# Kernel tuning notes

Hardware: AMD Instinct MI355X
Metric: run time of the kernel (lower is better)

The kernel has to match this reference:

```python
import jax, jax.numpy as jnp
import numpy as np

IN_FEATURES = 512
OUT_FEATURES = 64
INTER = 16
BATCH = 512


def setup_inputs() -> dict:
    key = jax.random.key(0)
    kx, kt = jax.random.split(key)
    x = jax.random.normal(kx, (BATCH, IN_FEATURES), dtype=jnp.float32)
    T = jax.random.normal(kt, (IN_FEATURES, OUT_FEATURES * INTER), dtype=jnp.float32)
    return {"x": x, "T": T}


def reference(x, T):
    B = x.shape[0]
    # M: [B, out, inter]
    M = (x @ T).reshape(B, OUT_FEATURES, INTER)
    # pairwise L1 distance over the intermediate dim: [B, B, out]
    l1 = jnp.sum(jnp.abs(M[:, None, :, :] - M[None, :, :, :]), axis=3)
    sim = jnp.exp(-l1)
    mask = 1.0 - jnp.eye(B, dtype=x.dtype)[:, :, None]  # exclude self
    o_b = jnp.sum(sim * mask, axis=1)  # [B, out]
    return jnp.concatenate([x, o_b], axis=1)
```

## Files before the change

### kernel.cpp

```cpp
#include <hip/hip_runtime.h>

#define IN_F 512
#define OUT_F 64
#define MCOLS 1024
#define OUT_STRIDE 576

__global__ __launch_bounds__(256) void gemm_init_kernel(
    const float* __restrict__ x, const float* __restrict__ T,
    float* __restrict__ M, float* __restrict__ out)
{
    __shared__ float xs[32][33];
    __shared__ float ts[32][64];

    const int tid = threadIdx.x;
    const int tx = tid & 15;
    const int ty = tid >> 4;
    const int c0 = blockIdx.x * 64;
    const int r0 = blockIdx.y * 32;

    float acc[2][4] = {{0.f,0.f,0.f,0.f},{0.f,0.f,0.f,0.f}};

    for (int kc = 0; kc < IN_F; kc += 32) {
        {
            const int ii = tid >> 3;
            const int kq = tid & 7;
            const float4 v = *(const float4*)(x + (r0 + ii) * IN_F + kc + kq * 4);
            xs[kq*4+0][ii] = v.x;
            xs[kq*4+1][ii] = v.y;
            xs[kq*4+2][ii] = v.z;
            xs[kq*4+3][ii] = v.w;
        }
        {
            const int jq = tid & 15;
#pragma unroll
            for (int h = 0; h < 2; ++h) {
                const int kk = (tid >> 4) + h * 16;
                const float4 v = *(const float4*)(T + (size_t)(kc + kk) * MCOLS + c0 + jq * 4);
                *(float4*)&ts[kk][jq * 4] = v;
            }
        }
        __syncthreads();
#pragma unroll
        for (int kk = 0; kk < 32; ++kk) {
            const float a0 = xs[kk][ty*2 + 0];
            const float a1 = xs[kk][ty*2 + 1];
            const float4 b = *(const float4*)&ts[kk][tx * 4];
            acc[0][0] += a0 * b.x; acc[0][1] += a0 * b.y;
            acc[0][2] += a0 * b.z; acc[0][3] += a0 * b.w;
            acc[1][0] += a1 * b.x; acc[1][1] += a1 * b.y;
            acc[1][2] += a1 * b.z; acc[1][3] += a1 * b.w;
        }
        __syncthreads();
    }

#pragma unroll
    for (int u = 0; u < 2; ++u) {
        const float4 w = make_float4(acc[u][0], acc[u][1], acc[u][2], acc[u][3]);
        *(float4*)(M + (size_t)(r0 + ty*2 + u) * MCOLS + c0 + tx * 4) = w;
    }

    const int bid = blockIdx.y * 16 + blockIdx.x;
    {
        const int idx = (bid * 256 + tid) * 4;
        const int i = idx >> 9;
        const int c = idx & 511;
        *(float4*)(out + (size_t)i * OUT_STRIDE + c) = *(const float4*)(x + idx);
    }
    if (tid < 128) {
        const int idx = bid * 128 + tid;
        const int i = idx >> 6;
        const int o = idx & 63;
        out[(size_t)i * OUT_STRIDE + IN_F + o] = -1.0f;
    }
}

__global__ __launch_bounds__(256) void pairwise_kernel(
    const float* __restrict__ M, float* __restrict__ out)
{
    __shared__ float sj[8 * 1024];

    const int tid = threadIdx.x;
    const int o  = tid & 63;
    const int ig = tid >> 6;
    const int it = blockIdx.x & 31;
    const int jc = blockIdx.x >> 5;
    const int i0 = it * 16;
    const int j0 = jc * 32;

    float mi[4][16];
#pragma unroll
    for (int r = 0; r < 4; ++r) {
        const float* rowp = M + (size_t)(i0 + ig*4 + r) * MCOLS + o * 16;
#pragma unroll
        for (int q = 0; q < 4; ++q) {
            const float4 v = *(const float4*)(rowp + q * 4);
            mi[r][q*4+0] = v.x; mi[r][q*4+1] = v.y;
            mi[r][q*4+2] = v.z; mi[r][q*4+3] = v.w;
        }
    }

    float acc[4] = {0.f, 0.f, 0.f, 0.f};

    const int ko = 4 * (tid & 3);
    const int oo = tid >> 2;

    for (int jb = 0; jb < 32; jb += 8) {
#pragma unroll
        for (int q = 0; q < 8; ++q) {
            const float4 v = *(const float4*)(M + (size_t)(j0 + jb + q) * MCOLS + tid * 4);
            float* s = sj + q * 1024 + oo;
            s[(ko+0)*64] = v.x;
            s[(ko+1)*64] = v.y;
            s[(ko+2)*64] = v.z;
            s[(ko+3)*64] = v.w;
        }
        __syncthreads();
#pragma unroll
        for (int q = 0; q < 8; ++q) {
            const float* s = sj + q * 1024 + o;
            float vj[16];
#pragma unroll
            for (int k = 0; k < 16; ++k) vj[k] = s[k * 64];
#pragma unroll
            for (int r = 0; r < 4; ++r) {
                float l1 = 0.f;
#pragma unroll
                for (int k = 0; k < 16; ++k) l1 += fabsf(mi[r][k] - vj[k]);
                acc[r] += __expf(-l1);
            }
        }
        __syncthreads();
    }

#pragma unroll
    for (int r = 0; r < 4; ++r) {
        atomicAdd(out + (size_t)(i0 + ig*4 + r) * OUT_STRIDE + IN_F + o, acc[r]);
    }
}

extern "C" void kernel_launch(void* const* d_in, const int* in_sizes, int n_in,
                              void* d_out, int out_size, void* d_ws, size_t ws_size,
                              hipStream_t stream) {
    const float* x = (const float*)d_in[0];
    const float* T = (const float*)d_in[1];
    float* out = (float*)d_out;
    float* M = (float*)d_ws;

    dim3 gridA(16, 16);
    gemm_init_kernel<<<gridA, 256, 0, stream>>>(x, T, M, out);
    pairwise_kernel<<<512, 256, 0, stream>>>(M, out);
}
```

Before: 98.25 us.

## Use bf16 MFMA GEMM with pre-transposed T and retile pairwise kernel

Measured after the change: 83.86 us. 14.6% less time.

```diff
diff --git a/kernel.cpp b/kernel.cpp
--- a/kernel.cpp
+++ b/kernel.cpp
@@ -1,141 +1,162 @@
 #include <hip/hip_runtime.h>
 
-#define IN_F 512
-#define OUT_F 64
-#define MCOLS 1024
 #define OUT_STRIDE 576
 
-__global__ __launch_bounds__(256) void gemm_init_kernel(
-    const float* __restrict__ x, const float* __restrict__ T,
-    float* __restrict__ M, float* __restrict__ out)
+typedef __attribute__((ext_vector_type(8))) short bf16x8;
+typedef __attribute__((ext_vector_type(4))) float f32x4;
+
+__device__ inline unsigned short f2bf(float f) {
+    unsigned u = __float_as_uint(f);
+    u = (u + 0x7FFFu + ((u >> 16) & 1u)) >> 16;
+    return (unsigned short)u;
+}
+
+__global__ __launch_bounds__(256) void transpose_T_kernel(
+    const float* __restrict__ T, unsigned short* __restrict__ Tb)
 {
-    __shared__ float xs[32][33];
-    __shared__ float ts[32][64];
-
-    const int tid = threadIdx.x;
-    const int tx = tid & 15;
-    const int ty = tid >> 4;
-    const int c0 = blockIdx.x * 64;
-    const int r0 = blockIdx.y * 32;
-
-    float acc[2][4] = {{0.f,0.f,0.f,0.f},{0.f,0.f,0.f,0.f}};
-
-    for (int kc = 0; kc < IN_F; kc += 32) {
-        {
-            const int ii = tid >> 3;
-            const int kq = tid & 7;
-            const float4 v = *(const float4*)(x + (r0 + ii) * IN_F + kc + kq * 4);
-            xs[kq*4+0][ii] = v.x;
-            xs[kq*4+1][ii] = v.y;
-            xs[kq*4+2][ii] = v.z;
-            xs[kq*4+3][ii] = v.w;
-        }
-        {
-            const int jq = tid & 15;
+    __shared__ float tt[64][68];
+    const int b = blockIdx.x;
+    const int t = threadIdx.x;
+    const int k0 = (b & 7) * 64, n0 = (b >> 3) * 64;
+    const int n4 = (t & 15) * 4, kr = t >> 4;
 #pragma unroll
-            for (int h = 0; h < 2; ++h) {
-                const int kk = (tid >> 4) + h * 16;
-                const float4 v = *(const float4*)(T + (size_t)(kc + kk) * MCOLS + c0 + jq * 4);
-                *(float4*)&ts[kk][jq * 4] = v;
-            }
-        }
-        __syncthreads();
+    for (int rr = 0; rr < 4; ++rr) {
+        const int k = rr * 16 + kr;
+        *(float4*)&tt[k][n4] = *(const float4*)(T + (size_t)(k0 + k) * 1024 + n0 + n4);
+    }
+    __syncthreads();
 #pragma unroll
-        for (int kk = 0; kk < 32; ++kk) {
-            const float a0 = xs[kk][ty*2 + 0];
-            const float a1 = xs[kk][ty*2 + 1];
-            const float4 b = *(const float4*)&ts[kk][tx * 4];
-            acc[0][0] += a0 * b.x; acc[0][1] += a0 * b.y;
-            acc[0][2] += a0 * b.z; acc[0][3] += a0 * b.w;
-            acc[1][0] += a1 * b.x; acc[1][1] += a1 * b.y;
-            acc[1][2] += a1 * b.z; acc[1][3] += a1 * b.w;
-        }
-        __syncthreads();
-    }
-
-#pragma unroll
-    for (int u = 0; u < 2; ++u) {
-        const float4 w = make_float4(acc[u][0], acc[u][1], acc[u][2], acc[u][3]);
-        *(float4*)(M + (size_t)(r0 + ty*2 + u) * MCOLS + c0 + tx * 4) = w;
-    }
-
-    const int bid = blockIdx.y * 16 + blockIdx.x;
-    {
-        const int idx = (bid * 256 + tid) * 4;
-        const int i = idx >> 9;
-        const int c = idx & 511;
-        *(float4*)(out + (size_t)i * OUT_STRIDE + c) = *(const float4*)(x + idx);
-    }
-    if (tid < 128) {
-        const int idx = bid * 128 + tid;
-        const int i = idx >> 6;
-        const int o = idx & 63;
-        out[(size_t)i * OUT_STRIDE + IN_F + o] = -1.0f;
+    for (int q = 0; q < 4; ++q) {
+        const int g = q * 256 + t;
+        const int nn = g >> 4, c = g & 15;
+        ushort4 w;
+        w.x = f2bf(tt[c * 4 + 0][nn]);
+        w.y = f2bf(tt[c * 4 + 1][nn]);
+        w.z = f2bf(tt[c * 4 + 2][nn]);
+        w.w = f2bf(tt[c * 4 + 3][nn]);
+        *(ushort4*)(Tb + (size_t)(n0 + nn) * 512 + k0 + c * 4) = w;
     }
 }
 
-__global__ __launch_bounds__(256) void pairwise_kernel(
+__global__ __launch_bounds__(256) void gemm_kernel(
+    const float* __restrict__ x, const unsigned short* __restrict__ Tb,
+    float* __restrict__ M, float* __restrict__ out)
+{
+    __shared__ unsigned short As[32 * 72];
+    __shared__ unsigned short Bs[64 * 72];
+    const int t = threadIdx.x;
+    const int bx = blockIdx.x & 15, by = blockIdx.x >> 4;
+    const int c0 = bx * 64, r0 = by * 32;
+    const int lane = t & 63, w = t >> 6;
+    const int m0 = (w >> 1) * 16, nb = (w & 1) * 32;
+    const int fl = lane & 15, q8 = (lane >> 4) * 8;
+    const int arow = t >> 3, k8 = (t & 7) * 8;
+
+    f32x4 acc0 = {0.f, 0.f, 0.f, 0.f}, acc1 = {0.f, 0.f, 0.f, 0.f};
+
+    for (int kc = 0; kc < 512; kc += 64) {
+        {
+            const float4 u = *(const float4*)(x + (size_t)(r0 + arow) * 512 + kc + k8);
+            const float4 v = *(const float4*)(x + (size_t)(r0 + arow) * 512 + kc + k8 + 4);
+            ushort4 w0, w1;
+            w0.x = f2bf(u.x); w0.y = f2bf(u.y); w0.z = f2bf(u.z); w0.w = f2bf(u.w);
+            w1.x = f2bf(v.x); w1.y = f2bf(v.y); w1.z = f2bf(v.z); w1.w = f2bf(v.w);
+            *(ushort4*)&As[arow * 72 + k8] = w0;
+            *(ushort4*)&As[arow * 72 + k8 + 4] = w1;
+        }
+#pragma unroll
+        for (int h = 0; h < 2; ++h) {
+            const int n = arow + h * 32;
+            *(uint4*)&Bs[n * 72 + k8] =
+                *(const uint4*)(Tb + (size_t)(c0 + n) * 512 + kc + k8);
+        }
+        __syncthreads();
+        const bf16x8 a0  = *(const bf16x8*)&As[(m0 + fl) * 72 + q8];
+        const bf16x8 a1  = *(const bf16x8*)&As[(m0 + fl) * 72 + 32 + q8];
+        const bf16x8 b00 = *(const bf16x8*)&Bs[(nb + fl) * 72 + q8];
+        const bf16x8 b01 = *(const bf16x8*)&Bs[(nb + fl) * 72 + 32 + q8];
+        const bf16x8 b10 = *(const bf16x8*)&Bs[(nb + 16 + fl) * 72 + q8];
+        const bf16x8 b11 = *(const bf16x8*)&Bs[(nb + 16 + fl) * 72 + 32 + q8];
+        acc0 = __builtin_amdgcn_mfma_f32_16x16x32_bf16(a0, b00, acc0, 0, 0, 0);
+        acc0 = __builtin_amdgcn_mfma_f32_16x16x32_bf16(a1, b01, acc0, 0, 0, 0);
+        acc1 = __builtin_amdgcn_mfma_f32_16x16x32_bf16(a0, b10, acc1, 0, 0, 0);
+        acc1 = __builtin_amdgcn_mfma_f32_16x16x32_bf16(a1, b11, acc1, 0, 0, 0);
+        __syncthreads();
+    }
+    const int orow = r0 + m0 + (lane >> 4) * 4;
+#pragma unroll
+    for (int r = 0; r < 4; ++r) {
+        M[(size_t)(orow + r) * 1024 + c0 + nb + fl]      = acc0[r];
+        M[(size_t)(orow + r) * 1024 + c0 + nb + 16 + fl] = acc1[r];
+    }
+
+    const int bid = blockIdx.x;
+    {
+        const int idx = (bid * 256 + t) * 4;
+        const int i = idx >> 9, c = idx & 511;
+        *(float4*)(out + (size_t)i * OUT_STRIDE + c) = *(const float4*)(x + idx);
+    }
+    if (t < 128) {
+        const int idx = bid * 128 + t;
+        const int i = idx >> 6, o = idx & 63;
+        out[(size_t)i * OUT_STRIDE + 512 + o] = -1.0f;
+    }
+}
+
+__global__ __launch_bounds__(256, 4) void pairwise_kernel(
     const float* __restrict__ M, float* __restrict__ out)
 {
-    __shared__ float sj[8 * 1024];
-
-    const int tid = threadIdx.x;
-    const int o  = tid & 63;
-    const int ig = tid >> 6;
-    const int it = blockIdx.x & 31;
-    const int jc = blockIdx.x >> 5;
-    const int i0 = it * 16;
-    const int j0 = jc * 32;
+    __shared__ float sj[8 * 1280];
+    const int t = threadIdx.x;
+    const int o = t & 63, ig = t >> 6;
+    const int it = blockIdx.x & 31, jc = blockIdx.x >> 5;
+    const int i0 = it * 16, j0 = jc * 16;
 
     float mi[4][16];
 #pragma unroll
     for (int r = 0; r < 4; ++r) {
-        const float* rowp = M + (size_t)(i0 + ig*4 + r) * MCOLS + o * 16;
+        const float* rp = M + (size_t)(i0 + ig * 4 + r) * 1024 + o * 16;
 #pragma unroll
         for (int q = 0; q < 4; ++q) {
-            const float4 v = *(const float4*)(rowp + q * 4);
-            mi[r][q*4+0] = v.x; mi[r][q*4+1] = v.y;
-            mi[r][q*4+2] = v.z; mi[r][q*4+3] = v.w;
+            const float4 v = *(const float4*)(rp + q * 4);
+            mi[r][q * 4 + 0] = v.x; mi[r][q * 4 + 1] = v.y;
+            mi[r][q * 4 + 2] = v.z; mi[r][q * 4 + 3] = v.w;
         }
     }
-
     float acc[4] = {0.f, 0.f, 0.f, 0.f};
 
-    const int ko = 4 * (tid & 3);
-    const int oo = tid >> 2;
-
-    for (int jb = 0; jb < 32; jb += 8) {
+    const int os = t >> 2, k4 = t & 3;
+#pragma unroll
+    for (int jb = 0; jb < 16; jb += 8) {
 #pragma unroll
         for (int q = 0; q < 8; ++q) {
-            const float4 v = *(const float4*)(M + (size_t)(j0 + jb + q) * MCOLS + tid * 4);
-            float* s = sj + q * 1024 + oo;
-            s[(ko+0)*64] = v.x;
-            s[(ko+1)*64] = v.y;
-            s[(ko+2)*64] = v.z;
-            s[(ko+3)*64] = v.w;
+            const float4 v = *(const float4*)(M + (size_t)(j0 + jb + q) * 1024 + t * 4);
+            *(float4*)&sj[q * 1280 + os * 20 + k4 * 4] = v;
         }
         __syncthreads();
 #pragma unroll
         for (int q = 0; q < 8; ++q) {
-            const float* s = sj + q * 1024 + o;
-            float vj[16];
+            const float* s = sj + q * 1280 + o * 20;
+            float l1[4] = {0.f, 0.f, 0.f, 0.f};
 #pragma unroll
-            for (int k = 0; k < 16; ++k) vj[k] = s[k * 64];
+            for (int q4 = 0; q4 < 4; ++q4) {
+                const float4 v = *(const float4*)(s + q4 * 4);
 #pragma unroll
-            for (int r = 0; r < 4; ++r) {
-                float l1 = 0.f;
+                for (int r = 0; r < 4; ++r) {
+                    l1[r] += fabsf(mi[r][q4 * 4 + 0] - v.x);
+                    l1[r] += fabsf(mi[r][q4 * 4 + 1] - v.y);
+                    l1[r] += fabsf(mi[r][q4 * 4 + 2] - v.z);
+                    l1[r] += fabsf(mi[r][q4 * 4 + 3] - v.w);
+                }
+            }
 #pragma unroll
-                for (int k = 0; k < 16; ++k) l1 += fabsf(mi[r][k] - vj[k]);
-                acc[r] += __expf(-l1);
-            }
+            for (int r = 0; r < 4; ++r) acc[r] += __expf(-l1[r]);
         }
         __syncthreads();
     }
-
 #pragma unroll
-    for (int r = 0; r < 4; ++r) {
-        atomicAdd(out + (size_t)(i0 + ig*4 + r) * OUT_STRIDE + IN_F + o, acc[r]);
-    }
+    for (int r = 0; r < 4; ++r)
+        atomicAdd(out + (size_t)(i0 + ig * 4 + r) * OUT_STRIDE + 512 + o, acc[r]);
 }
 
 extern "C" void kernel_launch(void* const* d_in, const int* in_sizes, int n_in,
@@ -145,8 +166,9 @@
     const float* T = (const float*)d_in[1];
     float* out = (float*)d_out;
     float* M = (float*)d_ws;
+    unsigned short* Tb = (unsigned short*)((char*)d_ws + (2 << 20));
 
-    dim3 gridA(16, 16);
-    gemm_init_kernel<<<gridA, 256, 0, stream>>>(x, T, M, out);
-    pairwise_kernel<<<512, 256, 0, stream>>>(M, out);
+    transpose_T_kernel<<<128, 256, 0, stream>>>(T, Tb);
+    gemm_kernel<<<256, 256, 0, stream>>>(x, Tb, M, out);
+    pairwise_kernel<<<1024, 256, 0, stream>>>(M, out);
 }
```
